# Optimization experiments

Measured on AMD Instinct MI355X. Metric: run time of the kernel, lower is better.

The kernel has to match this reference:

```python
import jax, jax.numpy as jnp
import numpy as np

EPS = 1e-5  # torch BatchNorm1d default eps


def _bn(x, gamma, beta):
    # training-mode batch norm over axis 0 (biased variance, like torch)
    m = x.mean(axis=0)
    v = x.var(axis=0)
    return (x - m) * jax.lax.rsqrt(v + EPS) * gamma + beta


def setup_inputs() -> dict:
    key = jax.random.key(0)
    ks = jax.random.split(key, 6)
    B, T, D_IN, E, H, D_OUT = 8192, 64, 2, 128, 128, 5
    s = 0.05
    f32 = jnp.float32
    return {
        "inputs": jax.random.normal(ks[0], (B, T, D_IN), f32),
        # input BatchNorm1d(2)
        "in_gamma": jnp.ones((D_IN,), f32),
        "in_beta": jnp.zeros((D_IN,), f32),
        # input embed MLP: Linear(2->128) + BN(128) + ReLU
        "W_emb": jax.random.normal(ks[1], (E, D_IN), f32) * s,
        "b_emb": jnp.zeros((E,), f32),
        "emb_gamma": jnp.ones((E,), f32),
        "emb_beta": jnp.zeros((E,), f32),
        # LSTMCell(128, 128): gate order i, f, g, o
        "W_ih": jax.random.normal(ks[2], (4 * H, E), f32) * s,
        "W_hh": jax.random.normal(ks[3], (4 * H, H), f32) * s,
        "b_ih": jnp.zeros((4 * H,), f32),
        "b_hh": jnp.zeros((4 * H,), f32),
        # output MLP: Linear(128->5) + BN(5), no activation
        "W_out": jax.random.normal(ks[4], (D_OUT, H), f32) * s,
        "b_out": jnp.zeros((D_OUT,), f32),
        "out_gamma": jnp.ones((D_OUT,), f32),
        "out_beta": jnp.zeros((D_OUT,), f32),
    }


def reference(inputs, in_gamma, in_beta, W_emb, b_emb, emb_gamma, emb_beta,
              W_ih, W_hh, b_ih, b_hh, W_out, b_out, out_gamma, out_beta):
    B, T, D = inputs.shape
    H = W_hh.shape[1]
    # input_norm over flattened (B*T, 2)
    x = _bn(inputs.reshape(-1, D), in_gamma, in_beta).reshape(B, T, D)

    h0 = jnp.zeros((B, H), inputs.dtype)
    c0 = jnp.zeros((B, H), inputs.dtype)

    def step(hc, x_t):
        h, c = hc
        # embed: Linear + BN + ReLU (per-step batch stats, as in torch loop)
        e = jax.nn.relu(_bn(x_t @ W_emb.T + b_emb, emb_gamma, emb_beta))
        gates = e @ W_ih.T + b_ih + h @ W_hh.T + b_hh
        i, f, g, o = jnp.split(gates, 4, axis=-1)
        c_new = jax.nn.sigmoid(f) * c + jax.nn.sigmoid(i) * jnp.tanh(g)
        h_new = jax.nn.sigmoid(o) * jnp.tanh(c_new)
        out = _bn(h_new @ W_out.T + b_out, out_gamma, out_beta)
        return (h_new, c_new), out

    (h, c), outs = jax.lax.scan(step, (h0, c0), jnp.swapaxes(x, 0, 1))
    return jnp.swapaxes(outs, 0, 1), (h, c)  # [B, T, 5], ([B,H],[B,H])
```

## Files before the change

### kernel.cpp

```cpp
#include <hip/hip_runtime.h>
#include <hip/hip_bf16.h>

#define BB 8192
#define TT 64
#define L2E 1.44269504088896f
#define LSTM_LDS_BYTES (98304 + 32768 + 16384)

typedef __attribute__((ext_vector_type(8))) short bf16x8;
typedef __attribute__((ext_vector_type(4))) float f32x4;

__device__ __forceinline__ float exp2g(float x) { return __builtin_amdgcn_exp2f(x); }
__device__ __forceinline__ float rcpg(float x)  { return __builtin_amdgcn_rcpf(x); }
__device__ __forceinline__ short f2bf_s(float x) {
  __hip_bfloat16 b = __float2bfloat16(x);
  return *reinterpret_cast<short*>(&b);
}
__device__ __forceinline__ int aidx(int row, int k) {
  return row * 512 + ((((k >> 3) ^ (row & 7))) << 3) + (k & 7);
}

__global__ void prep_stats_kernel(const float* __restrict__ Wih, const float* __restrict__ Whh,
                                  const float* __restrict__ bih, const float* __restrict__ bhh,
                                  const float* __restrict__ Wout,
                                  short* __restrict__ Wcb, short* __restrict__ Woutb,
                                  float* __restrict__ bc,
                                  const float* __restrict__ x, float* __restrict__ stats) {
  if (blockIdx.x < 67) {
    int idx = blockIdx.x * 256 + threadIdx.x;
    if (idx < 16384) {
      int l = idx & 63, f = idx >> 6;
      int kt = f >> 5, nt = f & 31;
      int k0 = kt * 32 + ((l >> 4) << 3);
      int col = nt * 16 + (l & 15);
      int gate = col >> 7;
      float s = (gate == 2) ? (2.f * L2E) : (-L2E);
      const float* src = (k0 < 128) ? (Wih + col * 128 + k0) : (Whh + col * 128 + (k0 - 128));
      bf16x8 v;
      #pragma unroll
      for (int e = 0; e < 8; e++) v[e] = f2bf_s(src[e] * s);
      *(bf16x8*)(Wcb + (size_t)idx * 8) = v;
    } else if (idx < 16640) {
      int i2 = idx - 16384;
      int l = i2 & 63, f = i2 >> 6;
      int k0 = f * 32 + ((l >> 4) << 3);
      int col = l & 15;
      bf16x8 v;
      #pragma unroll
      for (int e = 0; e < 8; e++)
        v[e] = (col < 5) ? f2bf_s(Wout[col * 128 + k0 + e]) : (short)0;
      *(bf16x8*)(Woutb + (size_t)i2 * 8) = v;
    } else {
      int i3 = idx - 16640;
      int gate = i3 >> 7;
      float s = (gate == 2) ? (2.f * L2E) : (-L2E);
      bc[i3] = (bih[i3] + bhh[i3]) * s;
    }
  } else {
    int t = blockIdx.x - 67, tid = threadIdx.x;
    float s0=0, s1=0, s2=0, s3=0, s4=0;
    for (int b = tid; b < BB; b += 256) {
      const float* p = x + ((size_t)b * TT + t) * 2;
      float x0 = p[0], x1 = p[1];
      s0 += x0; s1 += x1; s2 += x0*x0; s3 += x0*x1; s4 += x1*x1;
    }
    __shared__ float red[4][5];
    int lane = tid & 63, w = tid >> 6;
    #pragma unroll
    for (int off = 32; off > 0; off >>= 1) {
      s0 += __shfl_down(s0, off); s1 += __shfl_down(s1, off);
      s2 += __shfl_down(s2, off); s3 += __shfl_down(s3, off); s4 += __shfl_down(s4, off);
    }
    if (lane == 0) { red[w][0]=s0; red[w][1]=s1; red[w][2]=s2; red[w][3]=s3; red[w][4]=s4; }
    __syncthreads();
    if (tid < 5) stats[t*5 + tid] = red[0][tid] + red[1][tid] + red[2][tid] + red[3][tid];
  }
}

__global__ void coef_kernel(const float* __restrict__ stats,
                            const float* __restrict__ Wemb, const float* __restrict__ bemb,
                            const float* __restrict__ ing, const float* __restrict__ inb,
                            const float* __restrict__ eg, const float* __restrict__ eb,
                            float* __restrict__ A0, float* __restrict__ A1, float* __restrict__ Ct) {
  __shared__ float st[64][5];
  __shared__ float glob[4];
  int tid = threadIdx.x;
  for (int i = tid; i < 320; i += 128) st[i / 5][i % 5] = stats[i];
  __syncthreads();
  if (tid == 0) {
    float S0=0, S1=0, S00=0, S11=0;
    for (int t = 0; t < 64; t++) { S0+=st[t][0]; S1+=st[t][1]; S00+=st[t][2]; S11+=st[t][4]; }
    float inv_n = 1.f / (float)(BB * TT);
    float M0 = S0*inv_n, M1 = S1*inv_n;
    float V0 = S00*inv_n - M0*M0, V1 = S11*inv_n - M1*M1;
    float P0 = rsqrtf(V0 + 1e-5f) * ing[0];
    float P1 = rsqrtf(V1 + 1e-5f) * ing[1];
    glob[0]=P0; glob[1]=P1; glob[2]=inb[0]-M0*P0; glob[3]=inb[1]-M1*P1;
  }
  __syncthreads();
  float P0=glob[0], P1=glob[1], Q0=glob[2], Q1=glob[3];
  int j = tid;
  float w0 = Wemb[j*2], w1 = Wemb[j*2+1];
  float a0 = P0*w0, a1 = P1*w1;
  float cj = Q0*w0 + Q1*w1 + bemb[j];
  float gam = eg[j], bet = eb[j];
  float invB = 1.f / (float)BB;
  for (int t = 0; t < 64; t++) {
    float m0 = st[t][0]*invB, m1 = st[t][1]*invB;
    float v00 = st[t][2]*invB - m0*m0;
    float v01 = st[t][3]*invB - m0*m1;
    float v11 = st[t][4]*invB - m1*m1;
    float mean = a0*m0 + a1*m1 + cj;
    float var  = a0*a0*v00 + 2.f*a0*a1*v01 + a1*a1*v11;
    float G = rsqrtf(var + 1e-5f) * gam;
    A0[t*128 + j] = G * a0;
    A1[t*128 + j] = G * a1;
    Ct[t*128 + j] = G * cj + (bet - mean * G);
  }
}

__device__ __forceinline__ void write_e(short* acts_s, const float* tabs,
                                        int t, int er, int cg, const float* xs) {
  const float* a0p = tabs + t*128 + cg*8;
  const float* a1p = tabs + 8192 + t*128 + cg*8;
  const float* ccp = tabs + 16384 + t*128 + cg*8;
  const float4 a0a = *(const float4*)a0p, a0b = *(const float4*)(a0p + 4);
  const float4 a1a = *(const float4*)a1p, a1b = *(const float4*)(a1p + 4);
  const float4 cta = *(const float4*)ccp, ctb = *(const float4*)(ccp + 4);
  float x0 = xs[er * 128 + t * 2], x1 = xs[er * 128 + t * 2 + 1];
  bf16x8 v;
  v[0] = f2bf_s(fmaxf(fmaf(a0a.x, x0, fmaf(a1a.x, x1, cta.x)), 0.f));
  v[1] = f2bf_s(fmaxf(fmaf(a0a.y, x0, fmaf(a1a.y, x1, cta.y)), 0.f));
  v[2] = f2bf_s(fmaxf(fmaf(a0a.z, x0, fmaf(a1a.z, x1, cta.z)), 0.f));
  v[3] = f2bf_s(fmaxf(fmaf(a0a.w, x0, fmaf(a1a.w, x1, cta.w)), 0.f));
  v[4] = f2bf_s(fmaxf(fmaf(a0b.x, x0, fmaf(a1b.x, x1, ctb.x)), 0.f));
  v[5] = f2bf_s(fmaxf(fmaf(a0b.y, x0, fmaf(a1b.y, x1, ctb.y)), 0.f));
  v[6] = f2bf_s(fmaxf(fmaf(a0b.z, x0, fmaf(a1b.z, x1, ctb.z)), 0.f));
  v[7] = f2bf_s(fmaxf(fmaf(a0b.w, x0, fmaf(a1b.w, x1, ctb.w)), 0.f));
  int gk = (t & 1) * 16 + cg;
  *(bf16x8*)&acts_s[er * 512 + ((gk ^ (er & 7)) << 3)] = v;
}

__launch_bounds__(512, 1)
__global__ void lstm_kernel(const float* __restrict__ x,
                            const float* __restrict__ Atab,
                            const short* __restrict__ Wcb, const float* __restrict__ bc,
                            const short* __restrict__ Woutb, const float* __restrict__ bout,
                            float* __restrict__ outy, float* __restrict__ hout,
                            float* __restrict__ cout) {
  extern __shared__ __align__(16) char sm[];
  float* tabs   = (float*)sm;
  short* acts_s = (short*)(sm + 98304);
  float* xs     = (float*)(sm + 98304 + 32768);

  const int tid  = threadIdx.x;
  const int lane = tid & 63;
  const int w    = tid >> 6;
  const int row0 = blockIdx.x * 32;
  const int cl   = lane & 15;
  const int lq   = lane >> 4;
  const int er   = tid >> 4;
  const int cg   = tid & 15;

  {
    const float4* src = (const float4*)(x + (size_t)row0 * 128);
    float4* dst = (float4*)xs;
    dst[tid]       = src[tid];
    dst[tid + 512] = src[tid + 512];
    const float4* tsrc = (const float4*)Atab;
    float4* tdst = (float4*)tabs;
    #pragma unroll
    for (int i = 0; i < 12; i++) tdst[tid + i * 512] = tsrc[tid + i * 512];
  }

  float bgs[4];
  #pragma unroll
  for (int g = 0; g < 4; g++) bgs[g] = bc[g * 128 + w * 16 + cl];
  const float bov = (cl < 5) ? bout[cl] : 0.f;

  bf16x8 wreg[8][4];
  {
    const bf16x8* wptr = (const bf16x8*)Wcb;
    #pragma unroll
    for (int kt = 0; kt < 8; kt++)
      #pragma unroll
      for (int g = 0; g < 4; g++)
        wreg[kt][g] = wptr[(size_t)(kt * 32 + g * 8 + w) * 64 + lane];
  }
  bf16x8 wof[4];
  if ((w & 3) == 0) {
    #pragma unroll
    for (int kyt = 0; kyt < 4; kyt++)
      wof[kyt] = *(const bf16x8*)(Woutb + (size_t)(kyt * 64 + lane) * 8);
  }

  __syncthreads();

  write_e(acts_s, tabs, 0, er, cg, xs);
  {
    bf16x8 z = (bf16x8)0;
    int gk = 32 + 16 + cg;
    *(bf16x8*)&acts_s[er * 512 + ((gk ^ (er & 7)) << 3)] = z;
  }

  f32x4 cstate[2] = {{0.f,0.f,0.f,0.f},{0.f,0.f,0.f,0.f}};
  float hl[2][4];

  #pragma unroll 1
  for (int t = 0; t < TT; t++) {
    __syncthreads();
    const int ebuf = t & 1;
    const int hbuf = (t + 1) & 1;
    const bool do_y = ((w & 3) == 0) && (t > 0);

    f32x4 acc[4][2];
    #pragma unroll
    for (int g = 0; g < 4; g++)
      #pragma unroll
      for (int mt = 0; mt < 2; mt++)
        acc[g][mt] = (f32x4){bgs[g], bgs[g], bgs[g], bgs[g]};

    #pragma unroll
    for (int kt = 0; kt < 8; kt++) {
      int k = (kt < 4) ? (ebuf * 128 + (kt * 4 + lq) * 8)
                       : (256 + hbuf * 128 + ((kt - 4) * 4 + lq) * 8);
      bf16x8 a0 = *(const bf16x8*)&acts_s[aidx(cl, k)];
      #pragma unroll
      for (int g = 0; g < 4; g++)
        acc[g][0] = __builtin_amdgcn_mfma_f32_16x16x32_bf16(a0, wreg[kt][g], acc[g][0], 0, 0, 0);
    }
    #pragma unroll
    for (int kt = 0; kt < 8; kt++) {
      int k = (kt < 4) ? (ebuf * 128 + (kt * 4 + lq) * 8)
                       : (256 + hbuf * 128 + ((kt - 4) * 4 + lq) * 8);
      bf16x8 a1 = *(const bf16x8*)&acts_s[aidx(16 + cl, k)];
      #pragma unroll
      for (int g = 0; g < 4; g++)
        acc[g][1] = __builtin_amdgcn_mfma_f32_16x16x32_bf16(a1, wreg[kt][g], acc[g][1], 0, 0, 0);
    }

    f32x4 ya = (f32x4){0.f, 0.f, 0.f, 0.f};
    if (do_y) {
      int mty = w >> 2;
      int row = mty * 16 + cl;
      #pragma unroll
      for (int kyt = 0; kyt < 4; kyt++) {
        int k = 256 + hbuf * 128 + (kyt * 4 + lq) * 8;
        bf16x8 ah = *(const bf16x8*)&acts_s[aidx(row, k)];
        ya = __builtin_amdgcn_mfma_f32_16x16x32_bf16(ah, wof[kyt], ya, 0, 0, 0);
      }
    }

    if (t < TT - 1)
      write_e(acts_s, tabs, t + 1, er, cg, xs);

    #pragma unroll
    for (int mt = 0; mt < 2; mt++) {
      #pragma unroll
      for (int q = 0; q < 4; q++) {
        float Ei = exp2g(acc[0][mt][q]);
        float Ef = exp2g(acc[1][mt][q]);
        float Eg = exp2g(acc[2][mt][q]);
        float Eo = exp2g(acc[3][mt][q]);
        float di = 1.f + Ei, df = 1.f + Ef, dg = 1.f + Eg;
        float p  = di * dg;
        float num = fmaf(cstate[mt][q], p, (Eg - 1.f) * df);
        float cn  = num * rcpg(df * p);
        cstate[mt][q] = cn;
        float Ec = exp2g(cn * (2.f * L2E));
        float hn = (Ec - 1.f) * rcpg((1.f + Eo) * (1.f + Ec));
        hl[mt][q] = hn;
        int row = mt * 16 + lq * 4 + q;
        int k   = 256 + (t & 1) * 128 + w * 16 + cl;
        acts_s[aidx(row, k)] = f2bf_s(hn);
      }
    }

    if (do_y) {
      int mty = w >> 2;
      if (cl < 5) {
        #pragma unroll
        for (int q = 0; q < 4; q++) {
          int brow = row0 + mty * 16 + lq * 4 + q;
          outy[((size_t)brow * TT + (t - 1)) * 5 + cl] = ya[q] + bov;
        }
      }
    }
  }

  __syncthreads();
  if ((w & 3) == 0) {
    int mty = w >> 2;
    int row = mty * 16 + cl;
    f32x4 ya = (f32x4){0.f,0.f,0.f,0.f};
    #pragma unroll
    for (int kyt = 0; kyt < 4; kyt++) {
      int k = 256 + ((TT - 1) & 1) * 128 + (kyt * 4 + lq) * 8;
      bf16x8 ah = *(const bf16x8*)&acts_s[aidx(row, k)];
      ya = __builtin_amdgcn_mfma_f32_16x16x32_bf16(ah, wof[kyt], ya, 0, 0, 0);
    }
    if (cl < 5) {
      #pragma unroll
      for (int q = 0; q < 4; q++) {
        int brow = row0 + mty * 16 + lq * 4 + q;
        outy[((size_t)brow * TT + (TT - 1)) * 5 + cl] = ya[q] + bov;
      }
    }
  }

  #pragma unroll
  for (int mt = 0; mt < 2; mt++) {
    #pragma unroll
    for (int q = 0; q < 4; q++) {
      int brow = row0 + mt * 16 + lq * 4 + q;
      int col  = w * 16 + cl;
      hout[(size_t)brow * 128 + col] = hl[mt][q];
      cout[(size_t)brow * 128 + col] = cstate[mt][q];
    }
  }
}

__global__ void ostats_kernel(const float* __restrict__ outy, float* __restrict__ ostp) {
  int t = blockIdx.x >> 2, part = blockIdx.x & 3;
  int tid = threadIdx.x;
  float s[5] = {0,0,0,0,0}, s2[5] = {0,0,0,0,0};
  int b0 = part * 2048;
  for (int b = b0 + tid; b < b0 + 2048; b += 256) {
    const float* p = outy + ((size_t)b * TT + t) * 5;
    #pragma unroll
    for (int k = 0; k < 5; k++) { float v = p[k]; s[k] += v; s2[k] += v*v; }
  }
  __shared__ float red[4][10];
  int lane = tid & 63, w = tid >> 6;
  #pragma unroll
  for (int off = 32; off > 0; off >>= 1) {
    #pragma unroll
    for (int k = 0; k < 5; k++) {
      s[k]  += __shfl_down(s[k], off);
      s2[k] += __shfl_down(s2[k], off);
    }
  }
  if (lane == 0) {
    #pragma unroll
    for (int k = 0; k < 5; k++) { red[w][k] = s[k]; red[w][5+k] = s2[k]; }
  }
  __syncthreads();
  if (tid < 10) ostp[blockIdx.x * 10 + tid] = red[0][tid]+red[1][tid]+red[2][tid]+red[3][tid];
}

__global__ void onorm_kernel(float* __restrict__ outy, const float* __restrict__ ostp,
                             const float* __restrict__ og, const float* __restrict__ ob) {
  __shared__ float sc[320], sh[320];
  int tid = threadIdx.x;
  const float invB = 1.f / (float)BB;
  for (int i = tid; i < 320; i += 256) {
    int t = i / 5, k = i - t * 5;
    float m  = (ostp[(t*4+0)*10+k]   + ostp[(t*4+1)*10+k]   + ostp[(t*4+2)*10+k]   + ostp[(t*4+3)*10+k]) * invB;
    float s2 = (ostp[(t*4+0)*10+5+k] + ostp[(t*4+1)*10+5+k] + ostp[(t*4+2)*10+5+k] + ostp[(t*4+3)*10+5+k]) * invB;
    float v = s2 - m * m;
    float scale = rsqrtf(v + 1e-5f) * og[k];
    sc[i] = scale;
    sh[i] = ob[k] - m * scale;
  }
  __syncthreads();
  const int N = BB * TT * 5;
  for (int i = blockIdx.x * 256 + tid; i < N; i += gridDim.x * 256) {
    int j = i % 320;
    outy[i] = fmaf(outy[i], sc[j], sh[j]);
  }
}

extern "C" void kernel_launch(void* const* d_in, const int* in_sizes, int n_in,
                              void* d_out, int out_size, void* d_ws, size_t ws_size,
                              hipStream_t stream) {
  const float* xin  = (const float*)d_in[0];
  const float* ing  = (const float*)d_in[1];
  const float* inb  = (const float*)d_in[2];
  const float* Wemb = (const float*)d_in[3];
  const float* bemb = (const float*)d_in[4];
  const float* eg   = (const float*)d_in[5];
  const float* eb   = (const float*)d_in[6];
  const float* Wih  = (const float*)d_in[7];
  const float* Whh  = (const float*)d_in[8];
  const float* bih  = (const float*)d_in[9];
  const float* bhh  = (const float*)d_in[10];
  const float* Wout = (const float*)d_in[11];
  const float* bout = (const float*)d_in[12];
  const float* og   = (const float*)d_in[13];
  const float* ob   = (const float*)d_in[14];

  float* ws    = (float*)d_ws;
  float* stats = ws;
  float* A0    = ws + 1024;
  float* A1    = ws + 9216;
  float* Ct    = ws + 17408;
  float* bc    = ws + 25600;
  short* Wcb   = (short*)(ws + 26624);
  short* Woutb = (short*)(ws + 92160);
  float* ostp  = ws + 93184;

  float* outy = (float*)d_out;
  float* hout = outy + (size_t)BB * TT * 5;
  float* cout = hout + (size_t)BB * 128;

  hipFuncSetAttribute((const void*)lstm_kernel,
                      hipFuncAttributeMaxDynamicSharedMemorySize, LSTM_LDS_BYTES);

  prep_stats_kernel<<<131, 256, 0, stream>>>(Wih, Whh, bih, bhh, Wout, Wcb, Woutb, bc,
                                             xin, stats);
  coef_kernel <<<1, 128, 0, stream>>>(stats, Wemb, bemb, ing, inb, eg, eb, A0, A1, Ct);
  lstm_kernel <<<256, 512, LSTM_LDS_BYTES, stream>>>(xin, A0, Wcb, bc, Woutb, bout,
                                                     outy, hout, cout);
  ostats_kernel<<<256, 256, 0, stream>>>(outy, ostp);
  onorm_kernel <<<1024, 256, 0, stream>>>(outy, ostp, og, ob);
}
```

Baseline: 211.7 us.

## Fuse coefficient and output-stat kernels into LSTM kernel using atomics

The single-block coef_kernel is removed; each LSTM block now recomputes the per-timestep embed BN coefficients straight into LDS from the input stats. The ostats_kernel is removed by having the LSTM kernel reduce y sums and sums of squares per wave and atomically add them into a zeroed buffer, which onorm then reads directly. This saves two launches and a re-read of the output, at the cost of redundant per-block coefficient work, global atomics inside the time loop, and float atomics that make the result order non-deterministic.

Measured after the change: 293.5 us. +38.6%, slower.

```diff
diff --git a/kernel.cpp b/kernel.cpp
--- a/kernel.cpp
+++ b/kernel.cpp
@@ -24,7 +24,11 @@
                                   const float* __restrict__ Wout,
                                   short* __restrict__ Wcb, short* __restrict__ Woutb,
                                   float* __restrict__ bc,
-                                  const float* __restrict__ x, float* __restrict__ stats) {
+                                  const float* __restrict__ x, float* __restrict__ stats,
+                                  float* __restrict__ ostp) {
+  if (blockIdx.x == 0) {
+    for (int i = threadIdx.x; i < 640; i += 256) ostp[i] = 0.f;
+  }
   if (blockIdx.x < 67) {
     int idx = blockIdx.x * 256 + threadIdx.x;
     if (idx < 16384) {
@@ -73,48 +77,6 @@
     if (lane == 0) { red[w][0]=s0; red[w][1]=s1; red[w][2]=s2; red[w][3]=s3; red[w][4]=s4; }
     __syncthreads();
     if (tid < 5) stats[t*5 + tid] = red[0][tid] + red[1][tid] + red[2][tid] + red[3][tid];
-  }
-}
-
-__global__ void coef_kernel(const float* __restrict__ stats,
-                            const float* __restrict__ Wemb, const float* __restrict__ bemb,
-                            const float* __restrict__ ing, const float* __restrict__ inb,
-                            const float* __restrict__ eg, const float* __restrict__ eb,
-                            float* __restrict__ A0, float* __restrict__ A1, float* __restrict__ Ct) {
-  __shared__ float st[64][5];
-  __shared__ float glob[4];
-  int tid = threadIdx.x;
-  for (int i = tid; i < 320; i += 128) st[i / 5][i % 5] = stats[i];
-  __syncthreads();
-  if (tid == 0) {
-    float S0=0, S1=0, S00=0, S11=0;
-    for (int t = 0; t < 64; t++) { S0+=st[t][0]; S1+=st[t][1]; S00+=st[t][2]; S11+=st[t][4]; }
-    float inv_n = 1.f / (float)(BB * TT);
-    float M0 = S0*inv_n, M1 = S1*inv_n;
-    float V0 = S00*inv_n - M0*M0, V1 = S11*inv_n - M1*M1;
-    float P0 = rsqrtf(V0 + 1e-5f) * ing[0];
-    float P1 = rsqrtf(V1 + 1e-5f) * ing[1];
-    glob[0]=P0; glob[1]=P1; glob[2]=inb[0]-M0*P0; glob[3]=inb[1]-M1*P1;
-  }
-  __syncthreads();
-  float P0=glob[0], P1=glob[1], Q0=glob[2], Q1=glob[3];
-  int j = tid;
-  float w0 = Wemb[j*2], w1 = Wemb[j*2+1];
-  float a0 = P0*w0, a1 = P1*w1;
-  float cj = Q0*w0 + Q1*w1 + bemb[j];
-  float gam = eg[j], bet = eb[j];
-  float invB = 1.f / (float)BB;
-  for (int t = 0; t < 64; t++) {
-    float m0 = st[t][0]*invB, m1 = st[t][1]*invB;
-    float v00 = st[t][2]*invB - m0*m0;
-    float v01 = st[t][3]*invB - m0*m1;
-    float v11 = st[t][4]*invB - m1*m1;
-    float mean = a0*m0 + a1*m1 + cj;
-    float var  = a0*a0*v00 + 2.f*a0*a1*v01 + a1*a1*v11;
-    float G = rsqrtf(var + 1e-5f) * gam;
-    A0[t*128 + j] = G * a0;
-    A1[t*128 + j] = G * a1;
-    Ct[t*128 + j] = G * cj + (bet - mean * G);
   }
 }
 
@@ -142,11 +104,14 @@
 
 __launch_bounds__(512, 1)
 __global__ void lstm_kernel(const float* __restrict__ x,
-                            const float* __restrict__ Atab,
+                            const float* __restrict__ stats,
+                            const float* __restrict__ Wemb, const float* __restrict__ bemb,
+                            const float* __restrict__ ing, const float* __restrict__ inb,
+                            const float* __restrict__ eg, const float* __restrict__ eb,
                             const short* __restrict__ Wcb, const float* __restrict__ bc,
                             const short* __restrict__ Woutb, const float* __restrict__ bout,
                             float* __restrict__ outy, float* __restrict__ hout,
-                            float* __restrict__ cout) {
+                            float* __restrict__ cout, float* __restrict__ ostp) {
   extern __shared__ __align__(16) char sm[];
   float* tabs   = (float*)sm;
   short* acts_s = (short*)(sm + 98304);
@@ -161,17 +126,50 @@
   const int er   = tid >> 4;
   const int cg   = tid & 15;
 
+  for (int i = tid; i < 320; i += 512) xs[i] = stats[i];
+  __syncthreads();
+  if (tid == 0) {
+    float S0=0, S1=0, S00=0, S11=0;
+    for (int tt = 0; tt < 64; tt++) {
+      S0 += xs[tt*5]; S1 += xs[tt*5+1]; S00 += xs[tt*5+2]; S11 += xs[tt*5+4];
+    }
+    float inv_n = 1.f / (float)(BB * TT);
+    float M0 = S0*inv_n, M1 = S1*inv_n;
+    float V0 = S00*inv_n - M0*M0, V1 = S11*inv_n - M1*M1;
+    float P0 = rsqrtf(V0 + 1e-5f) * ing[0];
+    float P1 = rsqrtf(V1 + 1e-5f) * ing[1];
+    xs[320] = P0; xs[321] = P1; xs[322] = inb[0] - M0*P0; xs[323] = inb[1] - M1*P1;
+  }
+  __syncthreads();
+  {
+    float P0 = xs[320], P1 = xs[321], Q0 = xs[322], Q1 = xs[323];
+    int j = tid & 127, tg = tid >> 7;
+    float w0 = Wemb[j*2], w1 = Wemb[j*2+1];
+    float a0 = P0*w0, a1 = P1*w1;
+    float cj = Q0*w0 + Q1*w1 + bemb[j];
+    float gam = eg[j], bet = eb[j];
+    float invB = 1.f / (float)BB;
+    for (int tt = tg*16; tt < tg*16 + 16; tt++) {
+      float m0 = xs[tt*5]*invB, m1 = xs[tt*5+1]*invB;
+      float v00 = xs[tt*5+2]*invB - m0*m0;
+      float v01 = xs[tt*5+3]*invB - m0*m1;
+      float v11 = xs[tt*5+4]*invB - m1*m1;
+      float mean = a0*m0 + a1*m1 + cj;
+      float var  = a0*a0*v00 + 2.f*a0*a1*v01 + a1*a1*v11;
+      float G = rsqrtf(var + 1e-5f) * gam;
+      tabs[tt*128 + j]          = G * a0;
+      tabs[8192 + tt*128 + j]   = G * a1;
+      tabs[16384 + tt*128 + j]  = G * cj + (bet - mean * G);
+    }
+  }
+  __syncthreads();
+
   {
     const float4* src = (const float4*)(x + (size_t)row0 * 128);
     float4* dst = (float4*)xs;
     dst[tid]       = src[tid];
     dst[tid + 512] = src[tid + 512];
-    const float4* tsrc = (const float4*)Atab;
-    float4* tdst = (float4*)tabs;
-    #pragma unroll
-    for (int i = 0; i < 12; i++) tdst[tid + i * 512] = tsrc[tid + i * 512];
-  }
-
+  }
   float bgs[4];
   #pragma unroll
   for (int g = 0; g < 4; g++) bgs[g] = bc[g * 128 + w * 16 + cl];
@@ -277,12 +275,21 @@
 
     if (do_y) {
       int mty = w >> 2;
-      if (cl < 5) {
-        #pragma unroll
-        for (int q = 0; q < 4; q++) {
+      float ssum = 0.f, ssq = 0.f;
+      #pragma unroll
+      for (int q = 0; q < 4; q++) {
+        float v = ya[q] + bov;
+        if (cl < 5) {
           int brow = row0 + mty * 16 + lq * 4 + q;
-          outy[((size_t)brow * TT + (t - 1)) * 5 + cl] = ya[q] + bov;
+          outy[((size_t)brow * TT + (t - 1)) * 5 + cl] = v;
         }
+        ssum += v; ssq = fmaf(v, v, ssq);
+      }
+      ssum += __shfl_down(ssum, 32); ssq += __shfl_down(ssq, 32);
+      ssum += __shfl_down(ssum, 16); ssq += __shfl_down(ssq, 16);
+      if (lq == 0 && cl < 5) {
+        atomicAdd(&ostp[(t - 1) * 5 + cl], ssum);
+        atomicAdd(&ostp[320 + (t - 1) * 5 + cl], ssq);
       }
     }
   }
@@ -298,12 +305,21 @@
       bf16x8 ah = *(const bf16x8*)&acts_s[aidx(row, k)];
       ya = __builtin_amdgcn_mfma_f32_16x16x32_bf16(ah, wof[kyt], ya, 0, 0, 0);
     }
-    if (cl < 5) {
-      #pragma unroll
-      for (int q = 0; q < 4; q++) {
+    float ssum = 0.f, ssq = 0.f;
+    #pragma unroll
+    for (int q = 0; q < 4; q++) {
+      float v = ya[q] + bov;
+      if (cl < 5) {
         int brow = row0 + mty * 16 + lq * 4 + q;
-        outy[((size_t)brow * TT + (TT - 1)) * 5 + cl] = ya[q] + bov;
-      }
+        outy[((size_t)brow * TT + (TT - 1)) * 5 + cl] = v;
+      }
+      ssum += v; ssq = fmaf(v, v, ssq);
+    }
+    ssum += __shfl_down(ssum, 32); ssq += __shfl_down(ssq, 32);
+    ssum += __shfl_down(ssum, 16); ssq += __shfl_down(ssq, 16);
+    if (lq == 0 && cl < 5) {
+      atomicAdd(&ostp[(TT - 1) * 5 + cl], ssum);
+      atomicAdd(&ostp[320 + (TT - 1) * 5 + cl], ssq);
     }
   }
 
@@ -317,34 +333,6 @@
       cout[(size_t)brow * 128 + col] = cstate[mt][q];
     }
   }
-}
-
-__global__ void ostats_kernel(const float* __restrict__ outy, float* __restrict__ ostp) {
-  int t = blockIdx.x >> 2, part = blockIdx.x & 3;
-  int tid = threadIdx.x;
-  float s[5] = {0,0,0,0,0}, s2[5] = {0,0,0,0,0};
-  int b0 = part * 2048;
-  for (int b = b0 + tid; b < b0 + 2048; b += 256) {
-    const float* p = outy + ((size_t)b * TT + t) * 5;
-    #pragma unroll
-    for (int k = 0; k < 5; k++) { float v = p[k]; s[k] += v; s2[k] += v*v; }
-  }
-  __shared__ float red[4][10];
-  int lane = tid & 63, w = tid >> 6;
-  #pragma unroll
-  for (int off = 32; off > 0; off >>= 1) {
-    #pragma unroll
-    for (int k = 0; k < 5; k++) {
-      s[k]  += __shfl_down(s[k], off);
-      s2[k] += __shfl_down(s2[k], off);
-    }
-  }
-  if (lane == 0) {
-    #pragma unroll
-    for (int k = 0; k < 5; k++) { red[w][k] = s[k]; red[w][5+k] = s2[k]; }
-  }
-  __syncthreads();
-  if (tid < 10) ostp[blockIdx.x * 10 + tid] = red[0][tid]+red[1][tid]+red[2][tid]+red[3][tid];
 }
 
 __global__ void onorm_kernel(float* __restrict__ outy, const float* __restrict__ ostp,
@@ -354,8 +342,8 @@
   const float invB = 1.f / (float)BB;
   for (int i = tid; i < 320; i += 256) {
     int t = i / 5, k = i - t * 5;
-    float m  = (ostp[(t*4+0)*10+k]   + ostp[(t*4+1)*10+k]   + ostp[(t*4+2)*10+k]   + ostp[(t*4+3)*10+k]) * invB;
-    float s2 = (ostp[(t*4+0)*10+5+k] + ostp[(t*4+1)*10+5+k] + ostp[(t*4+2)*10+5+k] + ostp[(t*4+3)*10+5+k]) * invB;
+    float m  = ostp[i] * invB;
+    float s2 = ostp[320 + i] * invB;
     float v = s2 - m * m;
     float scale = rsqrtf(v + 1e-5f) * og[k];
     sc[i] = scale;
@@ -390,9 +378,6 @@
 
   float* ws    = (float*)d_ws;
   float* stats = ws;
-  float* A0    = ws + 1024;
-  float* A1    = ws + 9216;
-  float* Ct    = ws + 17408;
   float* bc    = ws + 25600;
   short* Wcb   = (short*)(ws + 26624);
   short* Woutb = (short*)(ws + 92160);
@@ -406,10 +391,9 @@
                       hipFuncAttributeMaxDynamicSharedMemorySize, LSTM_LDS_BYTES);
 
   prep_stats_kernel<<<131, 256, 0, stream>>>(Wih, Whh, bih, bhh, Wout, Wcb, Woutb, bc,
-                                             xin, stats);
-  coef_kernel <<<1, 128, 0, stream>>>(stats, Wemb, bemb, ing, inb, eg, eb, A0, A1, Ct);
-  lstm_kernel <<<256, 512, LSTM_LDS_BYTES, stream>>>(xin, A0, Wcb, bc, Woutb, bout,
-                                                     outy, hout, cout);
-  ostats_kernel<<<256, 256, 0, stream>>>(outy, ostp);
+                                             xin, stats, ostp);
+  lstm_kernel <<<256, 512, LSTM_LDS_BYTES, stream>>>(xin, stats, Wemb, bemb, ing, inb,
+                                                     eg, eb, Wcb, bc, Woutb, bout,
+                                                     outy, hout, cout, ostp);
   onorm_kernel <<<1024, 256, 0, stream>>>(outy, ostp, og, ob);
 }
```
